# Kernel tuning notes

Hardware: AMD Instinct MI355X
Metric: run time of the kernel (lower is better)

Reference implementation:

```python
import jax, jax.numpy as jnp
import numpy as np

B, NQ, NK, D, H, DR, MLPD = 32, 32, 4096, 256, 8, 2, 2048
ID = D // DR  # internal dim for downsampled cross-attention
EPS = 1e-5


def _ln(x, g, b):
    m = jnp.mean(x, -1, keepdims=True)
    v = jnp.mean((x - m) ** 2, -1, keepdims=True)
    return (x - m) / jnp.sqrt(v + EPS) * g + b


def _attn(q, k, v, qw, qb, kw, kb, vw, vb, ow, ob):
    # linear projections (weights stored as [in, out])
    q = q @ qw + qb
    k = k @ kw + kb
    v = v @ vw + vb
    b, nq, c = q.shape
    d = c // H
    qh = q.reshape(b, nq, H, d)
    kh = k.reshape(b, -1, H, d)
    vh = v.reshape(b, -1, H, d)
    scores = jnp.einsum('bqhd,bkhd->bhqk', qh, kh) * (1.0 / np.sqrt(d))
    a = jax.nn.softmax(scores, axis=-1)
    o = jnp.einsum('bhqk,bkhd->bqhd', a, vh).reshape(b, nq, c)
    return o @ ow + ob


def _forward(queries, keys, query_pe,
             sa_qw, sa_qb, sa_kw, sa_kb, sa_vw, sa_vb, sa_ow, sa_ob,
             t2i_qw, t2i_qb, t2i_kw, t2i_kb, t2i_vw, t2i_vb, t2i_ow, t2i_ob,
             i2t_qw, i2t_qb, i2t_kw, i2t_kb, i2t_vw, i2t_vb, i2t_ow, i2t_ob,
             mlp_w1, mlp_b1, mlp_w2, mlp_b2,
             ln1_g, ln1_b, ln2_g, ln2_b, ln3_g, ln3_b, ln4_g, ln4_b):
    # skip_first_layer_pe = False
    queries = queries + query_pe
    attn_out = _attn(queries, queries, queries,
                     sa_qw, sa_qb, sa_kw, sa_kb, sa_vw, sa_vb, sa_ow, sa_ob)
    queries = _ln(queries + attn_out, ln1_g, ln1_b)
    # cross attention: tokens -> image
    q = queries + query_pe
    attn_out = _attn(q, keys, keys,
                     t2i_qw, t2i_qb, t2i_kw, t2i_kb, t2i_vw, t2i_vb, t2i_ow, t2i_ob)
    queries = _ln(queries + attn_out, ln2_g, ln2_b)
    # MLP block (num_layers=1): act(x W1 + b1) W2 + b2, act = ReLU
    mlp_out = jax.nn.relu(queries @ mlp_w1 + mlp_b1) @ mlp_w2 + mlp_b2
    queries = _ln(queries + mlp_out, ln3_g, ln3_b)
    # cross attention: image -> tokens
    q = queries + query_pe
    attn_out = _attn(keys, q, queries,
                     i2t_qw, i2t_qb, i2t_kw, i2t_kb, i2t_vw, i2t_vb, i2t_ow, i2t_ob)
    keys = _ln(keys + attn_out, ln4_g, ln4_b)
    return queries, keys


def setup_inputs() -> dict:
    key = jax.random.key(0)
    ks = iter(jax.random.split(key, 64))
    def w(shape, s=0.02):
        return jax.random.normal(next(ks), shape, jnp.float32) * s
    inp = {
        'queries': w((B, NQ, D), 1.0),
        'keys': w((B, NK, D), 1.0),
        'query_pe': w((B, NQ, D), 1.0),
    }
    for pre, idim in [('sa', D), ('t2i', ID), ('i2t', ID)]:
        inp[pre + '_qw'] = w((D, idim)); inp[pre + '_qb'] = jnp.zeros((idim,), jnp.float32)
        inp[pre + '_kw'] = w((D, idim)); inp[pre + '_kb'] = jnp.zeros((idim,), jnp.float32)
        inp[pre + '_vw'] = w((D, idim)); inp[pre + '_vb'] = jnp.zeros((idim,), jnp.float32)
        inp[pre + '_ow'] = w((idim, D)); inp[pre + '_ob'] = jnp.zeros((D,), jnp.float32)
    inp['mlp_w1'] = w((D, MLPD)); inp['mlp_b1'] = jnp.zeros((MLPD,), jnp.float32)
    inp['mlp_w2'] = w((MLPD, D)); inp['mlp_b2'] = jnp.zeros((D,), jnp.float32)
    for i in range(1, 5):
        inp['ln%d_g' % i] = jnp.ones((D,), jnp.float32)
        inp['ln%d_b' % i] = jnp.zeros((D,), jnp.float32)
    return inp


def reference(queries, keys, query_pe,
              sa_qw, sa_qb, sa_kw, sa_kb, sa_vw, sa_vb, sa_ow, sa_ob,
              t2i_qw, t2i_qb, t2i_kw, t2i_kb, t2i_vw, t2i_vb, t2i_ow, t2i_ob,
              i2t_qw, i2t_qb, i2t_kw, i2t_kb, i2t_vw, i2t_vb, i2t_ow, i2t_ob,
              mlp_w1, mlp_b1, mlp_w2, mlp_b2,
              ln1_g, ln1_b, ln2_g, ln2_b, ln3_g, ln3_b, ln4_g, ln4_b):
    return _forward(queries, keys, query_pe,
                    sa_qw, sa_qb, sa_kw, sa_kb, sa_vw, sa_vb, sa_ow, sa_ob,
                    t2i_qw, t2i_qb, t2i_kw, t2i_kb, t2i_vw, t2i_vb, t2i_ow, t2i_ob,
                    i2t_qw, i2t_qb, i2t_kw, i2t_kb, i2t_vw, i2t_vb, i2t_ow, i2t_ob,
                    mlp_w1, mlp_b1, mlp_w2, mlp_b2,
                    ln1_g, ln1_b, ln2_g, ln2_b, ln3_g, ln3_b, ln4_g, ln4_b)
```

## Files before the change

### kernel.cpp

```cpp
#include <hip/hip_runtime.h>

typedef unsigned short u16;
typedef __attribute__((ext_vector_type(8))) short s16x8;
typedef __attribute__((ext_vector_type(4))) float f32x4;
typedef __attribute__((ext_vector_type(8))) unsigned short u16x8;

__device__ __forceinline__ float b2f(u16 u) {
  union { unsigned int i; float f; } v; v.i = ((unsigned int)u) << 16; return v.f;
}
__device__ __forceinline__ u16 f2b(float f) {
  union { float f; unsigned int i; } v; v.f = f;
  unsigned int r = v.i + 0x7FFFu + ((v.i >> 16) & 1u);
  return (u16)(r >> 16);
}
__device__ __forceinline__ int pk2(float a, float b) {
  return (int)f2b(a) | ((int)f2b(b) << 16);
}

template<bool RELU>
__global__ void __launch_bounds__(256) k_gemm(
    const u16* __restrict__ A, const u16* __restrict__ Wt,
    const float* __restrict__ bias, u16* __restrict__ C, int N, int K)
{
  __shared__ int4 smem4[2048];
  char* AsB = (char*)smem4;
  char* WsB = (char*)smem4 + 16384;
  const int t = threadIdx.x;
  const int lane = t & 63, wid = t >> 6;
  const int wm = wid >> 1, wn = wid & 1;
  const int l16 = lane & 15, lhi = lane >> 4;
  const int bCol = blockIdx.x * 128;
  const int bRow = blockIdx.y * 128;

  f32x4 acc[4][4];
#pragma unroll
  for (int i = 0; i < 4; ++i)
#pragma unroll
    for (int j = 0; j < 4; ++j) acc[i][j] = (f32x4){0.f, 0.f, 0.f, 0.f};

  const int nk = K >> 6;
  for (int kt = 0; kt < nk; ++kt) {
    const int k0 = kt << 6;
    int4 av[4], wv[4];
#pragma unroll
    for (int i = 0; i < 4; ++i) {
      int L = i * 4096 + t * 16;
      int r = L >> 7, cl = (L >> 4) & 7;
      av[i] = *(const int4*)(A + (size_t)(bRow + r) * K + k0 + cl * 8);
      wv[i] = *(const int4*)(Wt + (size_t)(bCol + r) * K + k0 + cl * 8);
    }
    if (kt) __syncthreads();
#pragma unroll
    for (int i = 0; i < 4; ++i) {
      int L = i * 4096 + t * 16;
      int r = L >> 7, cl = (L >> 4) & 7;
      int off = r * 128 + ((cl ^ (r & 7)) << 4);
      *(int4*)(AsB + off) = av[i];
      *(int4*)(WsB + off) = wv[i];
    }
    __syncthreads();
#pragma unroll
    for (int kk = 0; kk < 2; ++kk) {
      s16x8 af[4], bfr[4];
#pragma unroll
      for (int mt = 0; mt < 4; ++mt) {
        int r = wm * 64 + mt * 16 + l16;
        int ch = kk * 4 + lhi;
        af[mt] = *(const s16x8*)(AsB + r * 128 + ((ch ^ (r & 7)) << 4));
      }
#pragma unroll
      for (int nt = 0; nt < 4; ++nt) {
        int r = wn * 64 + nt * 16 + l16;
        int ch = kk * 4 + lhi;
        bfr[nt] = *(const s16x8*)(WsB + r * 128 + ((ch ^ (r & 7)) << 4));
      }
#pragma unroll
      for (int mt = 0; mt < 4; ++mt)
#pragma unroll
        for (int nt = 0; nt < 4; ++nt)
          acc[mt][nt] = __builtin_amdgcn_mfma_f32_16x16x32_bf16(
              af[mt], bfr[nt], acc[mt][nt], 0, 0, 0);
    }
  }
#pragma unroll
  for (int mt = 0; mt < 4; ++mt) {
#pragma unroll
    for (int nt = 0; nt < 4; ++nt) {
      int cg = bCol + wn * 64 + nt * 16 + l16;
      float bv = bias[cg];
#pragma unroll
      for (int rg = 0; rg < 4; ++rg) {
        int rgl = bRow + wm * 64 + mt * 16 + lhi * 4 + rg;
        float v = acc[mt][nt][rg] + bv;
        if (RELU) v = fmaxf(v, 0.f);
        C[(size_t)rgl * N + cg] = f2b(v);
      }
    }
  }
}

__global__ void __launch_bounds__(256) k_qphase1(
    const float* __restrict__ queries, const float* __restrict__ qpe,
    const u16* __restrict__ Wqkv,
    const float* __restrict__ bqkv,
    const u16* __restrict__ Wo,
    const float* __restrict__ ob,
    const float* __restrict__ g1, const float* __restrict__ b1,
    const u16* __restrict__ Wq2,
    const float* __restrict__ qb2,
    float* __restrict__ q1f, u16* __restrict__ qt)
{
  __shared__ float q0f[32][260];
  __shared__ u16 qkv[32][776];
  __shared__ u16 atb[32][264];
  __shared__ float rs[32][4], rq[32][4];
  const int b = blockIdx.x;
  const int t = threadIdx.x;
  const int lane = t & 63, w = t >> 6;
  const int l16 = lane & 15, lhi = lane >> 4;

  {
    const float4* qg = (const float4*)(queries + (size_t)b * 8192);
    const float4* pg = (const float4*)(qpe + (size_t)b * 8192);
    for (int i = t; i < 2048; i += 256) {
      int row = i >> 6, c4 = (i & 63) * 4;
      float4 qv = qg[i], pv = pg[i];
      *(float4*)&q0f[row][c4] =
          (float4){qv.x + pv.x, qv.y + pv.y, qv.z + pv.z, qv.w + pv.w};
    }
  }
  __syncthreads();

  {
    f32x4 acc[2][12];
#pragma unroll
    for (int i = 0; i < 2; ++i)
#pragma unroll
      for (int j = 0; j < 12; ++j) acc[i][j] = (f32x4){0.f, 0.f, 0.f, 0.f};
#pragma unroll
    for (int kk = 0; kk < 8; ++kk) {
      const int ko = kk * 32 + lhi * 8;
      s16x8 af[2], bfr[12];
#pragma unroll
      for (int mt = 0; mt < 2; ++mt) {
        const float* ap = &q0f[mt * 16 + l16][ko];
        float4 x = *(const float4*)ap;
        float4 y = *(const float4*)(ap + 4);
        int4 p = (int4){pk2(x.x, x.y), pk2(x.z, x.w),
                        pk2(y.x, y.y), pk2(y.z, y.w)};
        af[mt] = *(s16x8*)&p;
      }
#pragma unroll
      for (int nt = 0; nt < 12; ++nt) {
        int row = w * 192 + nt * 16 + l16;
        bfr[nt] = *(const s16x8*)(Wqkv + (size_t)row * 256 + ko);
      }
#pragma unroll
      for (int mt = 0; mt < 2; ++mt)
#pragma unroll
        for (int nt = 0; nt < 12; ++nt)
          acc[mt][nt] = __builtin_amdgcn_mfma_f32_16x16x32_bf16(
              af[mt], bfr[nt], acc[mt][nt], 0, 0, 0);
    }
#pragma unroll
    for (int mt = 0; mt < 2; ++mt)
#pragma unroll
      for (int nt = 0; nt < 12; ++nt) {
        int cg = w * 192 + nt * 16 + l16;
        float bv = bqkv[cg];
#pragma unroll
        for (int rg = 0; rg < 4; ++rg)
          qkv[mt * 16 + lhi * 4 + rg][cg] = f2b(acc[mt][nt][rg] + bv);
      }
  }
  __syncthreads();

  {
    int q = t >> 3, h = t & 7;
    float Qh[32];
#pragma unroll
    for (int c = 0; c < 4; ++c) {
      u16x8 v = *(const u16x8*)&qkv[q][h * 32 + c * 8];
#pragma unroll
      for (int e = 0; e < 8; ++e) Qh[c * 8 + e] = b2f(v[e]);
    }
    float s[32], mx = -INFINITY;
#pragma unroll 4
    for (int j = 0; j < 32; ++j) {
      float a = 0.f;
#pragma unroll
      for (int c = 0; c < 4; ++c) {
        u16x8 v = *(const u16x8*)&qkv[j][256 + h * 32 + c * 8];
#pragma unroll
        for (int e = 0; e < 8; ++e) a += Qh[c * 8 + e] * b2f(v[e]);
      }
      s[j] = a * 0.17677669529663687f;
      mx = fmaxf(mx, s[j]);
    }
    float sum = 0.f;
#pragma unroll
    for (int j = 0; j < 32; ++j) { s[j] = __expf(s[j] - mx); sum += s[j]; }
    float o[32];
#pragma unroll
    for (int d = 0; d < 32; ++d) o[d] = 0.f;
#pragma unroll 4
    for (int j = 0; j < 32; ++j) {
      float p = s[j];
#pragma unroll
      for (int c = 0; c < 4; ++c) {
        u16x8 v = *(const u16x8*)&qkv[j][512 + h * 32 + c * 8];
#pragma unroll
        for (int e = 0; e < 8; ++e) o[c * 8 + e] += p * b2f(v[e]);
      }
    }
    float inv = 1.f / sum;
#pragma unroll
    for (int d = 0; d < 32; ++d) atb[q][h * 32 + d] = f2b(o[d] * inv);
  }
  __syncthreads();

  float yv[2][4][4];
  {
    f32x4 acc[2][4];
#pragma unroll
    for (int i = 0; i < 2; ++i)
#pragma unroll
      for (int j = 0; j < 4; ++j) acc[i][j] = (f32x4){0.f, 0.f, 0.f, 0.f};
#pragma unroll
    for (int kk = 0; kk < 8; ++kk) {
      const int ko = kk * 32 + lhi * 8;
      s16x8 af[2], bfr[4];
#pragma unroll
      for (int mt = 0; mt < 2; ++mt)
        af[mt] = *(const s16x8*)&atb[mt * 16 + l16][ko];
#pragma unroll
      for (int nt = 0; nt < 4; ++nt) {
        int row = w * 64 + nt * 16 + l16;
        bfr[nt] = *(const s16x8*)(Wo + (size_t)row * 256 + ko);
      }
#pragma unroll
      for (int mt = 0; mt < 2; ++mt)
#pragma unroll
        for (int nt = 0; nt < 4; ++nt)
          acc[mt][nt] = __builtin_amdgcn_mfma_f32_16x16x32_bf16(
              af[mt], bfr[nt], acc[mt][nt], 0, 0, 0);
    }
#pragma unroll
    for (int mt = 0; mt < 2; ++mt) {
#pragma unroll
      for (int rg = 0; rg < 4; ++rg) {
        int row = mt * 16 + lhi * 4 + rg;
        float ps = 0.f, pq = 0.f;
#pragma unroll
        for (int nt = 0; nt < 4; ++nt) {
          int cg = w * 64 + nt * 16 + l16;
          float v = acc[mt][nt][rg] + ob[cg] + q0f[row][cg];
          yv[mt][nt][rg] = v;
          ps += v; pq += v * v;
        }
#pragma unroll
        for (int msk = 1; msk < 16; msk <<= 1) {
          ps += __shfl_xor(ps, msk);
          pq += __shfl_xor(pq, msk);
        }
        if (l16 == 0) { rs[row][w] = ps; rq[row][w] = pq; }
      }
    }
  }
  __syncthreads();
  {
#pragma unroll
    for (int mt = 0; mt < 2; ++mt) {
#pragma unroll
      for (int rg = 0; rg < 4; ++rg) {
        int row = mt * 16 + lhi * 4 + rg;
        float ts = rs[row][0] + rs[row][1] + rs[row][2] + rs[row][3];
        float tq = rq[row][0] + rq[row][1] + rq[row][2] + rq[row][3];
        float mean = ts * (1.f / 256.f);
        float var = tq * (1.f / 256.f) - mean * mean;
        float rstd = rsqrtf(var + 1e-5f);
#pragma unroll
        for (int nt = 0; nt < 4; ++nt) {
          int cg = w * 64 + nt * 16 + l16;
          float y = (yv[mt][nt][rg] - mean) * rstd * g1[cg] + b1[cg];
          size_t gi = ((size_t)b * 32 + row) * 256 + cg;
          q1f[gi] = y;
          atb[row][cg] = f2b(y + qpe[gi]);
        }
      }
    }
  }
  __syncthreads();

  {
    f32x4 acc[2][2];
#pragma unroll
    for (int i = 0; i < 2; ++i)
#pragma unroll
      for (int j = 0; j < 2; ++j) acc[i][j] = (f32x4){0.f, 0.f, 0.f, 0.f};
#pragma unroll
    for (int kk = 0; kk < 8; ++kk) {
      const int ko = kk * 32 + lhi * 8;
      s16x8 af[2], bfr[2];
#pragma unroll
      for (int mt = 0; mt < 2; ++mt)
        af[mt] = *(const s16x8*)&atb[mt * 16 + l16][ko];
#pragma unroll
      for (int nt = 0; nt < 2; ++nt) {
        int row = w * 32 + nt * 16 + l16;
        bfr[nt] = *(const s16x8*)(Wq2 + (size_t)row * 256 + ko);
      }
#pragma unroll
      for (int mt = 0; mt < 2; ++mt)
#pragma unroll
        for (int nt = 0; nt < 2; ++nt)
          acc[mt][nt] = __builtin_amdgcn_mfma_f32_16x16x32_bf16(
              af[mt], bfr[nt], acc[mt][nt], 0, 0, 0);
    }
#pragma unroll
    for (int mt = 0; mt < 2; ++mt)
#pragma unroll
      for (int nt = 0; nt < 2; ++nt) {
        int cg = w * 32 + nt * 16 + l16;
        float bv = qb2[cg];
#pragma unroll
        for (int rg = 0; rg < 4; ++rg) {
          int row = mt * 16 + lhi * 4 + rg;
          qt[((size_t)b * 32 + row) * 128 + cg] = f2b(acc[mt][nt][rg] + bv);
        }
      }
  }
}

__global__ void __launch_bounds__(512, 2) k_gemm_kvq(
    const float* __restrict__ A, const u16* __restrict__ Wt,
    const float* __restrict__ bias, u16* __restrict__ KV, u16* __restrict__ QB)
{
  __shared__ char smem[49152];
  char* AsB = smem;
  const int t = threadIdx.x;
  const int lane = t & 63, wid = t >> 6;
  const int wm = wid >> 2, wn = wid & 3;
  const int l16 = lane & 15, lhi = lane >> 4;
  const int bRow = blockIdx.x * 128;

  f32x4 acc[4][6];
#pragma unroll
  for (int i = 0; i < 4; ++i)
#pragma unroll
    for (int j = 0; j < 6; ++j) acc[i][j] = (f32x4){0.f, 0.f, 0.f, 0.f};

  for (int kt = 0; kt < 4; ++kt) {
    const int k0 = kt << 6;
    float4 a0r[2], a1r[2];
#pragma unroll
    for (int i = 0; i < 2; ++i) {
      int L = i * 8192 + t * 16;
      int r = L >> 7, cl = (L >> 4) & 7;
      const float* Af = A + (size_t)(bRow + r) * 256 + k0 + cl * 8;
      a0r[i] = *(const float4*)Af;
      a1r[i] = *(const float4*)(Af + 4);
    }
    if (kt) __syncthreads();
#pragma unroll
    for (int i = 0; i < 2; ++i) {
      int L = i * 8192 + t * 16;
      int r = L >> 7, cl = (L >> 4) & 7;
      int4 p = (int4){pk2(a0r[i].x, a0r[i].y), pk2(a0r[i].z, a0r[i].w),
                      pk2(a1r[i].x, a1r[i].y), pk2(a1r[i].z, a1r[i].w)};
      *(int4*)(AsB + r * 128 + ((cl ^ (r & 7)) << 4)) = p;
    }
    __syncthreads();
#pragma unroll
    for (int kk = 0; kk < 2; ++kk) {
      s16x8 af[4], bfr[6];
#pragma unroll
      for (int nt = 0; nt < 6; ++nt) {
        int row = wn * 96 + nt * 16 + l16;
        bfr[nt] = *(const s16x8*)(Wt + (size_t)row * 256 + k0 + kk * 32 + lhi * 8);
      }
#pragma unroll
      for (int mt = 0; mt < 4; ++mt) {
        int r = wm * 64 + mt * 16 + l16;
        int ch = kk * 4 + lhi;
        af[mt] = *(const s16x8*)(AsB + r * 128 + ((ch ^ (r & 7)) << 4));
      }
#pragma unroll
      for (int mt = 0; mt < 4; ++mt)
#pragma unroll
        for (int nt = 0; nt < 6; ++nt)
          acc[mt][nt] = __builtin_amdgcn_mfma_f32_16x16x32_bf16(
              af[mt], bfr[nt], acc[mt][nt], 0, 0, 0);
    }
  }
  u16* ldsO = (u16*)smem;
  for (int half = 0; half < 2; ++half) {
    __syncthreads();
    if (wm == half) {
#pragma unroll
      for (int mt = 0; mt < 4; ++mt) {
#pragma unroll
        for (int nt = 0; nt < 6; ++nt) {
          int cg = wn * 96 + nt * 16 + l16;
          float bv = bias[cg];
#pragma unroll
          for (int rg = 0; rg < 4; ++rg) {
            int r = mt * 16 + lhi * 4 + rg;
            ldsO[r * 384 + cg] = f2b(acc[mt][nt][rg] + bv);
          }
        }
      }
    }
    __syncthreads();
#pragma unroll
    for (int i = 0; i < 6; ++i) {
      int chunk = i * 512 + t;
      int r = chunk / 48, c8 = chunk - r * 48;
      int row = bRow + half * 64 + r;
      int4 v = *(int4*)(ldsO + r * 384 + c8 * 8);
      if (c8 < 32) *(int4*)(KV + (size_t)row * 256 + c8 * 8) = v;
      else         *(int4*)(QB + (size_t)row * 128 + (c8 - 32) * 8) = v;
    }
  }
}

__global__ void __launch_bounds__(256) k_gemm_ln(
    const u16* __restrict__ A, const u16* __restrict__ Wt,
    const float* __restrict__ bias, const float* __restrict__ res,
    const float* __restrict__ g, const float* __restrict__ bl,
    float* __restrict__ out)
{
  __shared__ int4 smem4[512];
  __shared__ float rsum[2][32][2], rsq[2][32][2];
  char* AsB = (char*)smem4;
  const int t = threadIdx.x;
  const int lane = t & 63, wid = t >> 6;
  const int wm = wid >> 1, wn = wid & 1;
  const int l16 = lane & 15, lhi = lane >> 4;
  const int bRow = blockIdx.x * 64;

  f32x4 acc[2][8];
#pragma unroll
  for (int i = 0; i < 2; ++i)
#pragma unroll
    for (int j = 0; j < 8; ++j) acc[i][j] = (f32x4){0.f, 0.f, 0.f, 0.f};

  for (int kt = 0; kt < 2; ++kt) {
    const int k0 = kt << 6;
    int4 av[2];
#pragma unroll
    for (int i = 0; i < 2; ++i) {
      int L = i * 4096 + t * 16;
      int r = L >> 7, cl = (L >> 4) & 7;
      av[i] = *(const int4*)(A + (size_t)(bRow + r) * 128 + k0 + cl * 8);
    }
    if (kt) __syncthreads();
#pragma unroll
    for (int i = 0; i < 2; ++i) {
      int L = i * 4096 + t * 16;
      int r = L >> 7, cl = (L >> 4) & 7;
      *(int4*)(AsB + r * 128 + ((cl ^ (r & 7)) << 4)) = av[i];
    }
    __syncthreads();
#pragma unroll
    for (int kk = 0; kk < 2; ++kk) {
      s16x8 af[2], bfr[8];
#pragma unroll
      for (int nt = 0; nt < 8; ++nt) {
        int row = wn * 128 + nt * 16 + l16;
        bfr[nt] = *(const s16x8*)(Wt + (size_t)row * 128 + k0 + kk * 32 + lhi * 8);
      }
#pragma unroll
      for (int mt = 0; mt < 2; ++mt) {
        int r = wm * 32 + mt * 16 + l16;
        int ch = kk * 4 + lhi;
        af[mt] = *(const s16x8*)(AsB + r * 128 + ((ch ^ (r & 7)) << 4));
      }
#pragma unroll
      for (int mt = 0; mt < 2; ++mt)
#pragma unroll
        for (int nt = 0; nt < 8; ++nt)
          acc[mt][nt] = __builtin_amdgcn_mfma_f32_16x16x32_bf16(
              af[mt], bfr[nt], acc[mt][nt], 0, 0, 0);
    }
  }
#pragma unroll
  for (int mt = 0; mt < 2; ++mt) {
#pragma unroll
    for (int nt = 0; nt < 8; ++nt) {
      int cg = wn * 128 + nt * 16 + l16;
      float bv = bias[cg];
#pragma unroll
      for (int rg = 0; rg < 4; ++rg) {
        int row = bRow + wm * 32 + mt * 16 + lhi * 4 + rg;
        acc[mt][nt][rg] += bv + res[(size_t)row * 256 + cg];
      }
    }
  }
#pragma unroll
  for (int mt = 0; mt < 2; ++mt) {
#pragma unroll
    for (int rg = 0; rg < 4; ++rg) {
      float ps = 0.f, pq = 0.f;
#pragma unroll
      for (int nt = 0; nt < 8; ++nt) {
        float v = acc[mt][nt][rg];
        ps += v; pq += v * v;
      }
#pragma unroll
      for (int msk = 1; msk < 16; msk <<= 1) {
        ps += __shfl_xor(ps, msk);
        pq += __shfl_xor(pq, msk);
      }
      if (l16 == 0) {
        int rl = mt * 16 + lhi * 4 + rg;
        rsum[wm][rl][wn] = ps;
        rsq[wm][rl][wn] = pq;
      }
    }
  }
  __syncthreads();
#pragma unroll
  for (int mt = 0; mt < 2; ++mt) {
#pragma unroll
    for (int rg = 0; rg < 4; ++rg) {
      int rl = mt * 16 + lhi * 4 + rg;
      float ts = rsum[wm][rl][0] + rsum[wm][rl][1];
      float tq = rsq[wm][rl][0] + rsq[wm][rl][1];
      float mean = ts * (1.f / 256.f);
      float var = tq * (1.f / 256.f) - mean * mean;
      float rstd = rsqrtf(var + 1e-5f);
      int row = bRow + wm * 32 + rl;
#pragma unroll
      for (int nt = 0; nt < 8; ++nt) {
        int cg = wn * 128 + nt * 16 + l16;
        out[(size_t)row * 256 + cg] =
            (acc[mt][nt][rg] - mean) * rstd * g[cg] + bl[cg];
      }
    }
  }
}

struct TDesc { const float* src; void* dst; int K; int N; int mode; int blk0; };
struct TArgs { TDesc d[24]; int n; };

__global__ void __launch_bounds__(256) k_trans(TArgs a)
{
  int blk = blockIdx.x;
  int i = 0;
  while (i + 1 < a.n && blk >= a.d[i + 1].blk0) ++i;
  TDesc td = a.d[i];
  int e = (blk - td.blk0) * 256 + threadIdx.x;
  int tot = td.K * td.N;
  if (e >= tot) return;
  if (td.mode == 0) {
    int k = e / td.N, n = e - k * td.N;
    ((u16*)td.dst)[(size_t)n * td.K + k] = f2b(td.src[e]);
  } else {
    ((float*)td.dst)[e] = td.src[e];
  }
}

__global__ void __launch_bounds__(128) k_attn_t2i_part(
    const u16* __restrict__ Qt, const u16* __restrict__ KV,
    float* __restrict__ part)
{
  __shared__ int4 kvs[4096];
  int c = blockIdx.x, b = blockIdx.y;
  int tid = threadIdx.x;
  const int4* src = (const int4*)(KV + ((size_t)b * 4096 + c * 128) * 256);
  for (int i = tid; i < 4096; i += 128) kvs[i] = src[i];
  __syncthreads();
  int qp = tid >> 3, h = tid & 7;
  const u16* lds = (const u16*)kvs;

  float q0[16], q1[16];
  {
    const u16* p0 = Qt + (size_t)(b * 32 + qp) * 128 + h * 16;
    const u16* p1 = Qt + (size_t)(b * 32 + qp + 16) * 128 + h * 16;
    u16x8 a0 = *(const u16x8*)p0, b0 = *(const u16x8*)(p0 + 8);
    u16x8 a1 = *(const u16x8*)p1, b1 = *(const u16x8*)(p1 + 8);
#pragma unroll
    for (int e = 0; e < 8; ++e) {
      q0[e] = b2f(a0[e]); q0[8 + e] = b2f(b0[e]);
      q1[e] = b2f(a1[e]); q1[8 + e] = b2f(b1[e]);
    }
  }
  float m0 = -INFINITY, s0 = 0.f, m1 = -INFINITY, s1 = 0.f;
  float acc0[16], acc1[16];
#pragma unroll
  for (int d = 0; d < 16; ++d) { acc0[d] = 0.f; acc1[d] = 0.f; }

  for (int j = 0; j < 128; ++j) {
    const u16* kr = lds + j * 256 + h * 16;
    u16x8 ka = *(const u16x8*)kr;
    u16x8 kb = *(const u16x8*)(kr + 8);
    float l0 = 0.f, l1 = 0.f;
#pragma unroll
    for (int e = 0; e < 8; ++e) {
      float klo = b2f(ka[e]), khi = b2f(kb[e]);
      l0 += q0[e] * klo + q0[8 + e] * khi;
      l1 += q1[e] * klo + q1[8 + e] * khi;
    }
    l0 *= 0.25f; l1 *= 0.25f;
    const u16* vr = kr + 128;
    u16x8 va = *(const u16x8*)vr;
    u16x8 vb = *(const u16x8*)(vr + 8);
    float nm0 = fmaxf(m0, l0), nm1 = fmaxf(m1, l1);
    float c0 = __expf(m0 - nm0), p0 = __expf(l0 - nm0);
    float c1 = __expf(m1 - nm1), p1 = __expf(l1 - nm1);
    s0 = s0 * c0 + p0; s1 = s1 * c1 + p1;
#pragma unroll
    for (int e = 0; e < 8; ++e) {
      float vlo = b2f(va[e]), vhi = b2f(vb[e]);
      acc0[e] = acc0[e] * c0 + p0 * vlo;
      acc0[8 + e] = acc0[8 + e] * c0 + p0 * vhi;
      acc1[e] = acc1[e] * c1 + p1 * vlo;
      acc1[8 + e] = acc1[8 + e] * c1 + p1 * vhi;
    }
    m0 = nm0; m1 = nm1;
  }
  float* r0 = part + (((size_t)(b * 32 + qp) * 8 + h) * 32 + c) * 18;
  float* r1 = part + (((size_t)(b * 32 + qp + 16) * 8 + h) * 32 + c) * 18;
#pragma unroll
  for (int d = 0; d < 16; ++d) { r0[d] = acc0[d]; r1[d] = acc1[d]; }
  r0[16] = m0; r0[17] = s0;
  r1[16] = m1; r1[17] = s1;
}

__global__ void __launch_bounds__(256) k_attn_t2i_merge(
    const float* __restrict__ part, u16* __restrict__ out)
{
  int b = blockIdx.x >> 3, h = blockIdx.x & 7;
  int q = threadIdx.x >> 3, ds = threadIdx.x & 7;
  const float* base = part + (((size_t)(b * 32 + q) * 8 + h) * 32) * 18;
  float mg = -INFINITY;
#pragma unroll 4
  for (int c = 0; c < 32; ++c) mg = fmaxf(mg, base[c * 18 + 16]);
  float sg = 0.f, a0 = 0.f, a1 = 0.f;
#pragma unroll 4
  for (int c = 0; c < 32; ++c) {
    const float* rec = base + c * 18;
    float w = __expf(rec[16] - mg);
    sg += rec[17] * w;
    a0 += rec[ds * 2] * w;
    a1 += rec[ds * 2 + 1] * w;
  }
  float inv = 1.f / sg;
  u16* op = out + (size_t)(b * 32 + q) * 128 + h * 16 + ds * 2;
  op[0] = f2b(a0 * inv);
  op[1] = f2b(a1 * inv);
}

__global__ void __launch_bounds__(256) k_attn_i2t(
    const u16* __restrict__ Qb, const u16* __restrict__ Kc,
    const u16* __restrict__ Vc, u16* __restrict__ out)
{
  __shared__ float Kl[32][132], Vl[32][132];
  int blk = blockIdx.x;
  int b = blk >> 7;
  int r0 = (blk & 127) * 32;
  for (int idx = threadIdx.x; idx < 4096; idx += 256) {
    int j = idx >> 7, c = idx & 127;
    Kl[j][c] = b2f(Kc[(size_t)(b * 32 + j) * 128 + c]);
    Vl[j][c] = b2f(Vc[(size_t)(b * 32 + j) * 128 + c]);
  }
  __syncthreads();
  int lr = threadIdx.x >> 3, h = threadIdx.x & 7;
  size_t row = (size_t)b * 4096 + r0 + lr;
  const u16* qp = Qb + row * 128 + h * 16;
  float q[16];
  {
    u16x8 qa = *(const u16x8*)qp;
    u16x8 qb2 = *(const u16x8*)(qp + 8);
#pragma unroll
    for (int e = 0; e < 8; ++e) { q[e] = b2f(qa[e]); q[8 + e] = b2f(qb2[e]); }
  }
  float lg[32];
  float mx = -INFINITY;
#pragma unroll
  for (int j = 0; j < 32; ++j) {
    float a = 0.f;
#pragma unroll
    for (int d = 0; d < 16; ++d) a += q[d] * Kl[j][h * 16 + d];
    lg[j] = a * 0.25f;
    mx = fmaxf(mx, lg[j]);
  }
  float sum = 0.f;
#pragma unroll
  for (int j = 0; j < 32; ++j) { lg[j] = __expf(lg[j] - mx); sum += lg[j]; }
  float acc[16];
#pragma unroll
  for (int d = 0; d < 16; ++d) acc[d] = 0.f;
#pragma unroll
  for (int j = 0; j < 32; ++j) {
    float p = lg[j];
#pragma unroll
    for (int d = 0; d < 16; ++d) acc[d] += p * Vl[j][h * 16 + d];
  }
  float inv = 1.f / sum;
  u16* op = out + row * 128 + h * 16;
#pragma unroll
  for (int d = 0; d < 16; ++d) op[d] = f2b(acc[d] * inv);
}

__global__ void __launch_bounds__(256) k_addln_small(
    const float* __restrict__ res, const u16* __restrict__ delta,
    const float* __restrict__ g, const float* __restrict__ bb,
    float* outf, u16* outb, const float* pe, u16* outpe)
{
  int row = blockIdx.x * 4 + (threadIdx.x >> 6);
  int lane = threadIdx.x & 63;
  size_t base = (size_t)row * 256 + lane * 4;
  float4 xv = *(const float4*)(res + base);
  ushort4 dv = *(const ushort4*)(delta + base);
  float v0 = xv.x + b2f(dv.x), v1 = xv.y + b2f(dv.y);
  float v2 = xv.z + b2f(dv.z), v3 = xv.w + b2f(dv.w);
  float sum = v0 + v1 + v2 + v3;
  float sq = v0 * v0 + v1 * v1 + v2 * v2 + v3 * v3;
#pragma unroll
  for (int msk = 1; msk < 64; msk <<= 1) {
    sum += __shfl_xor(sum, msk);
    sq += __shfl_xor(sq, msk);
  }
  float mean = sum * (1.f / 256.f);
  float var = sq * (1.f / 256.f) - mean * mean;
  float rstd = rsqrtf(var + 1e-5f);
  float4 gv = *(const float4*)(g + lane * 4);
  float4 bv = *(const float4*)(bb + lane * 4);
  float y0 = (v0 - mean) * rstd * gv.x + bv.x;
  float y1 = (v1 - mean) * rstd * gv.y + bv.y;
  float y2 = (v2 - mean) * rstd * gv.z + bv.z;
  float y3 = (v3 - mean) * rstd * gv.w + bv.w;
  if (outf) { float4 o{y0, y1, y2, y3}; *(float4*)(outf + base) = o; }
  if (outb) {
    ushort4 o{f2b(y0), f2b(y1), f2b(y2), f2b(y3)};
    *(ushort4*)(outb + base) = o;
  }
  if (outpe) {
    float4 pv = *(const float4*)(pe + base);
    ushort4 o{f2b(y0 + pv.x), f2b(y1 + pv.y), f2b(y2 + pv.z), f2b(y3 + pv.w)};
    *(ushort4*)(outpe + base) = o;
  }
}

extern "C" void kernel_launch(void* const* d_in, const int* in_sizes, int n_in,
                              void* d_out, int out_size, void* d_ws, size_t ws_size,
                              hipStream_t stream)
{
  (void)in_sizes; (void)n_in; (void)out_size; (void)ws_size;
  const float* queries = (const float*)d_in[0];
  const float* keys    = (const float*)d_in[1];
  const float* qpe     = (const float*)d_in[2];
  const float* sa_qw = (const float*)d_in[3];  const float* sa_qb = (const float*)d_in[4];
  const float* sa_kw = (const float*)d_in[5];  const float* sa_kb = (const float*)d_in[6];
  const float* sa_vw = (const float*)d_in[7];  const float* sa_vb = (const float*)d_in[8];
  const float* sa_ow = (const float*)d_in[9];  const float* sa_ob = (const float*)d_in[10];
  const float* t2i_qw = (const float*)d_in[11]; const float* t2i_qb = (const float*)d_in[12];
  const float* t2i_kw = (const float*)d_in[13]; const float* t2i_kb = (const float*)d_in[14];
  const float* t2i_vw = (const float*)d_in[15]; const float* t2i_vb = (const float*)d_in[16];
  const float* t2i_ow = (const float*)d_in[17]; const float* t2i_ob = (const float*)d_in[18];
  const float* i2t_qw = (const float*)d_in[19]; const float* i2t_qb = (const float*)d_in[20];
  const float* i2t_kw = (const float*)d_in[21]; const float* i2t_kb = (const float*)d_in[22];
  const float* i2t_vw = (const float*)d_in[23]; const float* i2t_vb = (const float*)d_in[24];
  const float* i2t_ow = (const float*)d_in[25]; const float* i2t_ob = (const float*)d_in[26];
  const float* mlp_w1 = (const float*)d_in[27]; const float* mlp_b1 = (const float*)d_in[28];
  const float* mlp_w2 = (const float*)d_in[29]; const float* mlp_b2 = (const float*)d_in[30];
  const float* ln1_g = (const float*)d_in[31]; const float* ln1_b = (const float*)d_in[32];
  const float* ln2_g = (const float*)d_in[33]; const float* ln2_b = (const float*)d_in[34];
  const float* ln3_g = (const float*)d_in[35]; const float* ln3_b = (const float*)d_in[36];
  const float* ln4_g = (const float*)d_in[37]; const float* ln4_b = (const float*)d_in[38];

  float* out_q = (float*)d_out;
  float* out_k = out_q + 262144;

  u16* kvbuf  = (u16*)out_k;
  u16* qb_big = (u16*)out_k + 33554432;
  float* t2i_part = (float*)((u16*)out_k + 50331648);

  char* ws = (char*)d_ws;
  size_t off = 0;
  auto alloc = [&](size_t bytes) -> char* {
    char* p = ws + off;
    off += (bytes + 255) & ~(size_t)255;
    return p;
  };
  u16* wt_saqkv = (u16*)alloc(768 * 256 * 2);
  u16* wt_saow  = (u16*)alloc(256 * 256 * 2);
  u16* wt_t2iq  = (u16*)alloc(128 * 256 * 2);
  u16* wt_kvq   = (u16*)alloc(384 * 256 * 2);
  u16* wt_t2io  = (u16*)alloc(256 * 128 * 2);
  u16* wt_i2tk  = (u16*)alloc(128 * 256 * 2);
  u16* wt_i2tv  = (u16*)alloc(128 * 256 * 2);
  u16* wt_i2to  = (u16*)alloc(256 * 128 * 2);
  u16* wt_w1    = (u16*)alloc(2048 * 256 * 2);
  u16* wt_w2    = (u16*)alloc(256 * 2048 * 2);
  float* b_saqkv = (float*)alloc(768 * 4);
  float* b_kvq   = (float*)alloc(384 * 4);
  float* q1f = (float*)alloc(262144 * 4);
  float* q2f = (float*)alloc(262144 * 4);
  u16* qt    = (u16*)alloc(131072 * 2);
  u16* at2   = (u16*)alloc(131072 * 2);
  u16* o2    = (u16*)alloc(262144 * 2);
  u16* q2b   = (u16*)alloc(262144 * 2);
  u16* hbuf  = (u16*)alloc(2097152 * 2);
  u16* mo    = (u16*)alloc(262144 * 2);
  u16* q3b   = (u16*)alloc(262144 * 2);
  u16* q3pe  = (u16*)alloc(262144 * 2);
  u16* kc    = (u16*)alloc(131072 * 2);
  u16* vc    = (u16*)alloc(131072 * 2);
  u16* ab_big = (u16*)alloc((size_t)16777216 * 2);

  TArgs ta{};
  int nb = 0, id = 0;
  auto addT = [&](const float* s, void* d, int K, int N, int mode) {
    ta.d[id].src = s; ta.d[id].dst = d; ta.d[id].K = K; ta.d[id].N = N;
    ta.d[id].mode = mode; ta.d[id].blk0 = nb;
    nb += (K * N + 255) / 256;
    ++id;
  };
  addT(sa_qw, wt_saqkv, 256, 256, 0);
  addT(sa_kw, wt_saqkv + 256 * 256, 256, 256, 0);
  addT(sa_vw, wt_saqkv + 512 * 256, 256, 256, 0);
  addT(sa_ow, wt_saow, 256, 256, 0);
  addT(t2i_qw, wt_t2iq, 256, 128, 0);
  addT(t2i_kw, wt_kvq, 256, 128, 0);
  addT(t2i_vw, wt_kvq + 128 * 256, 256, 128, 0);
  addT(i2t_qw, wt_kvq + 256 * 256, 256, 128, 0);
  addT(t2i_ow, wt_t2io, 128, 256, 0);
  addT(i2t_kw, wt_i2tk, 256, 128, 0);
  addT(i2t_vw, wt_i2tv, 256, 128, 0);
  addT(i2t_ow, wt_i2to, 128, 256, 0);
  addT(mlp_w1, wt_w1, 256, 2048, 0);
  addT(mlp_w2, wt_w2, 2048, 256, 0);
  addT(sa_qb, b_saqkv, 1, 256, 1);
  addT(sa_kb, b_saqkv + 256, 1, 256, 1);
  addT(sa_vb, b_saqkv + 512, 1, 256, 1);
  addT(t2i_kb, b_kvq, 1, 128, 1);
  addT(t2i_vb, b_kvq + 128, 1, 128, 1);
  addT(i2t_qb, b_kvq + 256, 1, 128, 1);
  ta.n = id;
  k_trans<<<nb, 256, 0, stream>>>(ta);

  k_qphase1<<<32, 256, 0, stream>>>(queries, qpe, wt_saqkv, b_saqkv,
                                    wt_saow, sa_ob, ln1_g, ln1_b,
                                    wt_t2iq, t2i_qb, q1f, qt);
  k_gemm_kvq<<<1024, 512, 0, stream>>>(keys, wt_kvq, b_kvq, kvbuf, qb_big);
  k_attn_t2i_part<<<dim3(32, 32), 128, 0, stream>>>(qt, kvbuf, t2i_part);
  k_attn_t2i_merge<<<256, 256, 0, stream>>>(t2i_part, at2);
  k_gemm<false><<<dim3(2, 8), 256, 0, stream>>>(at2, wt_t2io, t2i_ob,
                                                o2, 256, 128);
  k_addln_small<<<256, 256, 0, stream>>>(q1f, o2, ln2_g, ln2_b, q2f, q2b,
                                         nullptr, nullptr);
  k_gemm<true><<<dim3(16, 8), 256, 0, stream>>>(q2b, wt_w1, mlp_b1,
                                                hbuf, 2048, 256);
  k_gemm<false><<<dim3(2, 8), 256, 0, stream>>>(hbuf, wt_w2, mlp_b2,
                                                mo, 256, 2048);
  k_addln_small<<<256, 256, 0, stream>>>(q2f, mo, ln3_g, ln3_b, out_q, q3b,
                                         qpe, q3pe);
  k_gemm<false><<<dim3(1, 8), 256, 0, stream>>>(q3pe, wt_i2tk, i2t_kb,
                                                kc, 128, 256);
  k_gemm<false><<<dim3(1, 8), 256, 0, stream>>>(q3b, wt_i2tv, i2t_vb,
                                                vc, 128, 256);
  k_attn_i2t<<<4096, 256, 0, stream>>>(qb_big, kc, vc, ab_big);
  k_gemm_ln<<<2048, 256, 0, stream>>>(ab_big, wt_i2to, i2t_ob, keys,
                                      ln4_g, ln4_b, out_k);
}
```

Before: 550.9 us.

## Fuse t2i out-proj, LN2, MLP, LN3 and i2t K/V projections per batch

Replaces the chain of small GEMM and add-layernorm launches after token-to-image attention with a single per-batch kernel. It computes the output projection, residual plus LN2, the MLP in hidden-dimension chunks staged in LDS, residual plus LN3, and the image-to-token K and V projections. This removes several launches and global round-trips of intermediates. In exchange, the work runs on only 32 blocks, each streaming the full MLP weights from global memory.

Result: faster. 494.2 us (-10.3%).

```diff
diff --git a/kernel.cpp b/kernel.cpp
--- a/kernel.cpp
+++ b/kernel.cpp
@@ -15,88 +15,6 @@
 }
 __device__ __forceinline__ int pk2(float a, float b) {
   return (int)f2b(a) | ((int)f2b(b) << 16);
-}
-
-template<bool RELU>
-__global__ void __launch_bounds__(256) k_gemm(
-    const u16* __restrict__ A, const u16* __restrict__ Wt,
-    const float* __restrict__ bias, u16* __restrict__ C, int N, int K)
-{
-  __shared__ int4 smem4[2048];
-  char* AsB = (char*)smem4;
-  char* WsB = (char*)smem4 + 16384;
-  const int t = threadIdx.x;
-  const int lane = t & 63, wid = t >> 6;
-  const int wm = wid >> 1, wn = wid & 1;
-  const int l16 = lane & 15, lhi = lane >> 4;
-  const int bCol = blockIdx.x * 128;
-  const int bRow = blockIdx.y * 128;
-
-  f32x4 acc[4][4];
-#pragma unroll
-  for (int i = 0; i < 4; ++i)
-#pragma unroll
-    for (int j = 0; j < 4; ++j) acc[i][j] = (f32x4){0.f, 0.f, 0.f, 0.f};
-
-  const int nk = K >> 6;
-  for (int kt = 0; kt < nk; ++kt) {
-    const int k0 = kt << 6;
-    int4 av[4], wv[4];
-#pragma unroll
-    for (int i = 0; i < 4; ++i) {
-      int L = i * 4096 + t * 16;
-      int r = L >> 7, cl = (L >> 4) & 7;
-      av[i] = *(const int4*)(A + (size_t)(bRow + r) * K + k0 + cl * 8);
-      wv[i] = *(const int4*)(Wt + (size_t)(bCol + r) * K + k0 + cl * 8);
-    }
-    if (kt) __syncthreads();
-#pragma unroll
-    for (int i = 0; i < 4; ++i) {
-      int L = i * 4096 + t * 16;
-      int r = L >> 7, cl = (L >> 4) & 7;
-      int off = r * 128 + ((cl ^ (r & 7)) << 4);
-      *(int4*)(AsB + off) = av[i];
-      *(int4*)(WsB + off) = wv[i];
-    }
-    __syncthreads();
-#pragma unroll
-    for (int kk = 0; kk < 2; ++kk) {
-      s16x8 af[4], bfr[4];
-#pragma unroll
-      for (int mt = 0; mt < 4; ++mt) {
-        int r = wm * 64 + mt * 16 + l16;
-        int ch = kk * 4 + lhi;
-        af[mt] = *(const s16x8*)(AsB + r * 128 + ((ch ^ (r & 7)) << 4));
-      }
-#pragma unroll
-      for (int nt = 0; nt < 4; ++nt) {
-        int r = wn * 64 + nt * 16 + l16;
-        int ch = kk * 4 + lhi;
-        bfr[nt] = *(const s16x8*)(WsB + r * 128 + ((ch ^ (r & 7)) << 4));
-      }
-#pragma unroll
-      for (int mt = 0; mt < 4; ++mt)
-#pragma unroll
-        for (int nt = 0; nt < 4; ++nt)
-          acc[mt][nt] = __builtin_amdgcn_mfma_f32_16x16x32_bf16(
-              af[mt], bfr[nt], acc[mt][nt], 0, 0, 0);
-    }
-  }
-#pragma unroll
-  for (int mt = 0; mt < 4; ++mt) {
-#pragma unroll
-    for (int nt = 0; nt < 4; ++nt) {
-      int cg = bCol + wn * 64 + nt * 16 + l16;
-      float bv = bias[cg];
-#pragma unroll
-      for (int rg = 0; rg < 4; ++rg) {
-        int rgl = bRow + wm * 64 + mt * 16 + lhi * 4 + rg;
-        float v = acc[mt][nt][rg] + bv;
-        if (RELU) v = fmaxf(v, 0.f);
-        C[(size_t)rgl * N + cg] = f2b(v);
-      }
-    }
-  }
 }
 
 __global__ void __launch_bounds__(256) k_qphase1(
@@ -332,6 +250,279 @@
   }
 }
 
+__global__ void __launch_bounds__(256) k_qphase2(
+    const u16* __restrict__ at2,
+    const float* __restrict__ q1f,
+    const u16* __restrict__ Wo2,
+    const float* __restrict__ ob2,
+    const float* __restrict__ g2, const float* __restrict__ b2v,
+    const u16* __restrict__ W1,
+    const float* __restrict__ bb1,
+    const u16* __restrict__ W2,
+    const float* __restrict__ bb2,
+    const float* __restrict__ g3, const float* __restrict__ b3v,
+    const float* __restrict__ qpe,
+    const u16* __restrict__ Wk,
+    const float* __restrict__ kb,
+    const u16* __restrict__ Wv,
+    const float* __restrict__ vbv,
+    float* __restrict__ out_q, u16* __restrict__ kc, u16* __restrict__ vc)
+{
+  __shared__ u16 atb[32][136];
+  __shared__ float q2f[32][260];
+  __shared__ u16 q2b[32][264];
+  __shared__ u16 hb[32][520];
+  __shared__ u16 yb[32][264];
+  __shared__ u16 ypeb[32][264];
+  __shared__ float rs[32][4], rq[32][4];
+  const int b = blockIdx.x;
+  const int t = threadIdx.x;
+  const int lane = t & 63, w = t >> 6;
+  const int l16 = lane & 15, lhi = lane >> 4;
+
+  {
+    const int4* src = (const int4*)(at2 + (size_t)b * 32 * 128);
+    for (int i = t; i < 512; i += 256) {
+      int r = i >> 4, c8 = i & 15;
+      *(int4*)&atb[r][c8 * 8] = src[i];
+    }
+  }
+  __syncthreads();
+
+  {
+    f32x4 acc[2][4];
+#pragma unroll
+    for (int i = 0; i < 2; ++i)
+#pragma unroll
+      for (int j = 0; j < 4; ++j) acc[i][j] = (f32x4){0.f, 0.f, 0.f, 0.f};
+#pragma unroll
+    for (int kk = 0; kk < 4; ++kk) {
+      const int ko = kk * 32 + lhi * 8;
+      s16x8 af[2], bfr[4];
+#pragma unroll
+      for (int mt = 0; mt < 2; ++mt)
+        af[mt] = *(const s16x8*)&atb[mt * 16 + l16][ko];
+#pragma unroll
+      for (int nt = 0; nt < 4; ++nt) {
+        int row = w * 64 + nt * 16 + l16;
+        bfr[nt] = *(const s16x8*)(Wo2 + (size_t)row * 128 + ko);
+      }
+#pragma unroll
+      for (int mt = 0; mt < 2; ++mt)
+#pragma unroll
+        for (int nt = 0; nt < 4; ++nt)
+          acc[mt][nt] = __builtin_amdgcn_mfma_f32_16x16x32_bf16(
+              af[mt], bfr[nt], acc[mt][nt], 0, 0, 0);
+    }
+    float yv[2][4][4];
+#pragma unroll
+    for (int mt = 0; mt < 2; ++mt) {
+#pragma unroll
+      for (int rg = 0; rg < 4; ++rg) {
+        int row = mt * 16 + lhi * 4 + rg;
+        float ps = 0.f, pq = 0.f;
+#pragma unroll
+        for (int nt = 0; nt < 4; ++nt) {
+          int cg = w * 64 + nt * 16 + l16;
+          float v = acc[mt][nt][rg] + ob2[cg] +
+                    q1f[((size_t)b * 32 + row) * 256 + cg];
+          yv[mt][nt][rg] = v;
+          ps += v; pq += v * v;
+        }
+#pragma unroll
+        for (int msk = 1; msk < 16; msk <<= 1) {
+          ps += __shfl_xor(ps, msk);
+          pq += __shfl_xor(pq, msk);
+        }
+        if (l16 == 0) { rs[row][w] = ps; rq[row][w] = pq; }
+      }
+    }
+    __syncthreads();
+#pragma unroll
+    for (int mt = 0; mt < 2; ++mt) {
+#pragma unroll
+      for (int rg = 0; rg < 4; ++rg) {
+        int row = mt * 16 + lhi * 4 + rg;
+        float ts = rs[row][0] + rs[row][1] + rs[row][2] + rs[row][3];
+        float tq = rq[row][0] + rq[row][1] + rq[row][2] + rq[row][3];
+        float mean = ts * (1.f / 256.f);
+        float var = tq * (1.f / 256.f) - mean * mean;
+        float rstd = rsqrtf(var + 1e-5f);
+#pragma unroll
+        for (int nt = 0; nt < 4; ++nt) {
+          int cg = w * 64 + nt * 16 + l16;
+          float y = (yv[mt][nt][rg] - mean) * rstd * g2[cg] + b2v[cg];
+          q2f[row][cg] = y;
+          q2b[row][cg] = f2b(y);
+        }
+      }
+    }
+  }
+  __syncthreads();
+
+  f32x4 oacc[2][4];
+#pragma unroll
+  for (int i = 0; i < 2; ++i)
+#pragma unroll
+    for (int j = 0; j < 4; ++j) oacc[i][j] = (f32x4){0.f, 0.f, 0.f, 0.f};
+  for (int hc = 0; hc < 4; ++hc) {
+    f32x4 a1[2][8];
+#pragma unroll
+    for (int i = 0; i < 2; ++i)
+#pragma unroll
+      for (int j = 0; j < 8; ++j) a1[i][j] = (f32x4){0.f, 0.f, 0.f, 0.f};
+#pragma unroll
+    for (int kk = 0; kk < 8; ++kk) {
+      const int ko = kk * 32 + lhi * 8;
+      s16x8 af[2], bfr[8];
+#pragma unroll
+      for (int mt = 0; mt < 2; ++mt)
+        af[mt] = *(const s16x8*)&q2b[mt * 16 + l16][ko];
+#pragma unroll
+      for (int nt = 0; nt < 8; ++nt) {
+        int row = hc * 512 + w * 128 + nt * 16 + l16;
+        bfr[nt] = *(const s16x8*)(W1 + (size_t)row * 256 + ko);
+      }
+#pragma unroll
+      for (int mt = 0; mt < 2; ++mt)
+#pragma unroll
+        for (int nt = 0; nt < 8; ++nt)
+          a1[mt][nt] = __builtin_amdgcn_mfma_f32_16x16x32_bf16(
+              af[mt], bfr[nt], a1[mt][nt], 0, 0, 0);
+    }
+    if (hc) __syncthreads();
+#pragma unroll
+    for (int mt = 0; mt < 2; ++mt)
+#pragma unroll
+      for (int nt = 0; nt < 8; ++nt) {
+        int cg = w * 128 + nt * 16 + l16;
+        float bv = bb1[hc * 512 + cg];
+#pragma unroll
+        for (int rg = 0; rg < 4; ++rg)
+          hb[mt * 16 + lhi * 4 + rg][cg] =
+              f2b(fmaxf(a1[mt][nt][rg] + bv, 0.f));
+      }
+    __syncthreads();
+#pragma unroll
+    for (int kk2 = 0; kk2 < 16; ++kk2) {
+      const int ko = kk2 * 32 + lhi * 8;
+      s16x8 af[2], bfr[4];
+#pragma unroll
+      for (int mt = 0; mt < 2; ++mt)
+        af[mt] = *(const s16x8*)&hb[mt * 16 + l16][ko];
+#pragma unroll
+      for (int nt = 0; nt < 4; ++nt) {
+        int row = w * 64 + nt * 16 + l16;
+        bfr[nt] = *(const s16x8*)(W2 + (size_t)row * 2048 + hc * 512 + ko);
+      }
+#pragma unroll
+      for (int mt = 0; mt < 2; ++mt)
+#pragma unroll
+        for (int nt = 0; nt < 4; ++nt)
+          oacc[mt][nt] = __builtin_amdgcn_mfma_f32_16x16x32_bf16(
+              af[mt], bfr[nt], oacc[mt][nt], 0, 0, 0);
+    }
+  }
+
+  {
+    float yv[2][4][4];
+#pragma unroll
+    for (int mt = 0; mt < 2; ++mt) {
+#pragma unroll
+      for (int rg = 0; rg < 4; ++rg) {
+        int row = mt * 16 + lhi * 4 + rg;
+        float ps = 0.f, pq = 0.f;
+#pragma unroll
+        for (int nt = 0; nt < 4; ++nt) {
+          int cg = w * 64 + nt * 16 + l16;
+          float v = oacc[mt][nt][rg] + bb2[cg] + q2f[row][cg];
+          yv[mt][nt][rg] = v;
+          ps += v; pq += v * v;
+        }
+#pragma unroll
+        for (int msk = 1; msk < 16; msk <<= 1) {
+          ps += __shfl_xor(ps, msk);
+          pq += __shfl_xor(pq, msk);
+        }
+        if (l16 == 0) { rs[row][w] = ps; rq[row][w] = pq; }
+      }
+    }
+    __syncthreads();
+#pragma unroll
+    for (int mt = 0; mt < 2; ++mt) {
+#pragma unroll
+      for (int rg = 0; rg < 4; ++rg) {
+        int row = mt * 16 + lhi * 4 + rg;
+        float ts = rs[row][0] + rs[row][1] + rs[row][2] + rs[row][3];
+        float tq = rq[row][0] + rq[row][1] + rq[row][2] + rq[row][3];
+        float mean = ts * (1.f / 256.f);
+        float var = tq * (1.f / 256.f) - mean * mean;
+        float rstd = rsqrtf(var + 1e-5f);
+#pragma unroll
+        for (int nt = 0; nt < 4; ++nt) {
+          int cg = w * 64 + nt * 16 + l16;
+          float y = (yv[mt][nt][rg] - mean) * rstd * g3[cg] + b3v[cg];
+          size_t gi = ((size_t)b * 32 + row) * 256 + cg;
+          out_q[gi] = y;
+          yb[row][cg] = f2b(y);
+          ypeb[row][cg] = f2b(y + qpe[gi]);
+        }
+      }
+    }
+  }
+  __syncthreads();
+
+  {
+    f32x4 ak[2][2], av[2][2];
+#pragma unroll
+    for (int i = 0; i < 2; ++i)
+#pragma unroll
+      for (int j = 0; j < 2; ++j) {
+        ak[i][j] = (f32x4){0.f, 0.f, 0.f, 0.f};
+        av[i][j] = (f32x4){0.f, 0.f, 0.f, 0.f};
+      }
+#pragma unroll
+    for (int kk = 0; kk < 8; ++kk) {
+      const int ko = kk * 32 + lhi * 8;
+      s16x8 afk[2], afv[2], bk[2], bv2[2];
+#pragma unroll
+      for (int mt = 0; mt < 2; ++mt) {
+        afk[mt] = *(const s16x8*)&ypeb[mt * 16 + l16][ko];
+        afv[mt] = *(const s16x8*)&yb[mt * 16 + l16][ko];
+      }
+#pragma unroll
+      for (int nt = 0; nt < 2; ++nt) {
+        int row = w * 32 + nt * 16 + l16;
+        bk[nt] = *(const s16x8*)(Wk + (size_t)row * 256 + ko);
+        bv2[nt] = *(const s16x8*)(Wv + (size_t)row * 256 + ko);
+      }
+#pragma unroll
+      for (int mt = 0; mt < 2; ++mt)
+#pragma unroll
+        for (int nt = 0; nt < 2; ++nt) {
+          ak[mt][nt] = __builtin_amdgcn_mfma_f32_16x16x32_bf16(
+              afk[mt], bk[nt], ak[mt][nt], 0, 0, 0);
+          av[mt][nt] = __builtin_amdgcn_mfma_f32_16x16x32_bf16(
+              afv[mt], bv2[nt], av[mt][nt], 0, 0, 0);
+        }
+    }
+#pragma unroll
+    for (int mt = 0; mt < 2; ++mt)
+#pragma unroll
+      for (int nt = 0; nt < 2; ++nt) {
+        int cg = w * 32 + nt * 16 + l16;
+        float kbv = kb[cg], vbb = vbv[cg];
+#pragma unroll
+        for (int rg = 0; rg < 4; ++rg) {
+          int row = mt * 16 + lhi * 4 + rg;
+          size_t gi = ((size_t)b * 32 + row) * 128 + cg;
+          kc[gi] = f2b(ak[mt][nt][rg] + kbv);
+          vc[gi] = f2b(av[mt][nt][rg] + vbb);
+        }
+      }
+  }
+}
+
 __global__ void __launch_bounds__(512, 2) k_gemm_kvq(
     const float* __restrict__ A, const u16* __restrict__ Wt,
     const float* __restrict__ bias, u16* __restrict__ KV, u16* __restrict__ QB)
@@ -702,46 +893,6 @@
   u16* op = out + row * 128 + h * 16;
 #pragma unroll
   for (int d = 0; d < 16; ++d) op[d] = f2b(acc[d] * inv);
-}
-
-__global__ void __launch_bounds__(256) k_addln_small(
-    const float* __restrict__ res, const u16* __restrict__ delta,
-    const float* __restrict__ g, const float* __restrict__ bb,
-    float* outf, u16* outb, const float* pe, u16* outpe)
-{
-  int row = blockIdx.x * 4 + (threadIdx.x >> 6);
-  int lane = threadIdx.x & 63;
-  size_t base = (size_t)row * 256 + lane * 4;
-  float4 xv = *(const float4*)(res + base);
-  ushort4 dv = *(const ushort4*)(delta + base);
-  float v0 = xv.x + b2f(dv.x), v1 = xv.y + b2f(dv.y);
-  float v2 = xv.z + b2f(dv.z), v3 = xv.w + b2f(dv.w);
-  float sum = v0 + v1 + v2 + v3;
-  float sq = v0 * v0 + v1 * v1 + v2 * v2 + v3 * v3;
-#pragma unroll
-  for (int msk = 1; msk < 64; msk <<= 1) {
-    sum += __shfl_xor(sum, msk);
-    sq += __shfl_xor(sq, msk);
-  }
-  float mean = sum * (1.f / 256.f);
-  float var = sq * (1.f / 256.f) - mean * mean;
-  float rstd = rsqrtf(var + 1e-5f);
-  float4 gv = *(const float4*)(g + lane * 4);
-  float4 bv = *(const float4*)(bb + lane * 4);
-  float y0 = (v0 - mean) * rstd * gv.x + bv.x;
-  float y1 = (v1 - mean) * rstd * gv.y + bv.y;
-  float y2 = (v2 - mean) * rstd * gv.z + bv.z;
-  float y3 = (v3 - mean) * rstd * gv.w + bv.w;
-  if (outf) { float4 o{y0, y1, y2, y3}; *(float4*)(outf + base) = o; }
-  if (outb) {
-    ushort4 o{f2b(y0), f2b(y1), f2b(y2), f2b(y3)};
-    *(ushort4*)(outb + base) = o;
-  }
-  if (outpe) {
-    float4 pv = *(const float4*)(pe + base);
-    ushort4 o{f2b(y0 + pv.x), f2b(y1 + pv.y), f2b(y2 + pv.z), f2b(y3 + pv.w)};
-    *(ushort4*)(outpe + base) = o;
-  }
 }
 
 extern "C" void kernel_launch(void* const* d_in, const int* in_sizes, int n_in,
@@ -798,15 +949,8 @@
   float* b_saqkv = (float*)alloc(768 * 4);
   float* b_kvq   = (float*)alloc(384 * 4);
   float* q1f = (float*)alloc(262144 * 4);
-  float* q2f = (float*)alloc(262144 * 4);
   u16* qt    = (u16*)alloc(131072 * 2);
   u16* at2   = (u16*)alloc(131072 * 2);
-  u16* o2    = (u16*)alloc(262144 * 2);
-  u16* q2b   = (u16*)alloc(262144 * 2);
-  u16* hbuf  = (u16*)alloc(2097152 * 2);
-  u16* mo    = (u16*)alloc(262144 * 2);
-  u16* q3b   = (u16*)alloc(262144 * 2);
-  u16* q3pe  = (u16*)alloc(262144 * 2);
   u16* kc    = (u16*)alloc(131072 * 2);
   u16* vc    = (u16*)alloc(131072 * 2);
   u16* ab_big = (u16*)alloc((size_t)16777216 * 2);
@@ -848,20 +992,11 @@
   k_gemm_kvq<<<1024, 512, 0, stream>>>(keys, wt_kvq, b_kvq, kvbuf, qb_big);
   k_attn_t2i_part<<<dim3(32, 32), 128, 0, stream>>>(qt, kvbuf, t2i_part);
   k_attn_t2i_merge<<<256, 256, 0, stream>>>(t2i_part, at2);
-  k_gemm<false><<<dim3(2, 8), 256, 0, stream>>>(at2, wt_t2io, t2i_ob,
-                                                o2, 256, 128);
-  k_addln_small<<<256, 256, 0, stream>>>(q1f, o2, ln2_g, ln2_b, q2f, q2b,
-                                         nullptr, nullptr);
-  k_gemm<true><<<dim3(16, 8), 256, 0, stream>>>(q2b, wt_w1, mlp_b1,
-                                                hbuf, 2048, 256);
-  k_gemm<false><<<dim3(2, 8), 256, 0, stream>>>(hbuf, wt_w2, mlp_b2,
-                                                mo, 256, 2048);
-  k_addln_small<<<256, 256, 0, stream>>>(q2f, mo, ln3_g, ln3_b, out_q, q3b,
-                                         qpe, q3pe);
-  k_gemm<false><<<dim3(1, 8), 256, 0, stream>>>(q3pe, wt_i2tk, i2t_kb,
-                                                kc, 128, 256);
-  k_gemm<false><<<dim3(1, 8), 256, 0, stream>>>(q3b, wt_i2tv, i2t_vb,
-                                                vc, 128, 256);
+  k_qphase2<<<32, 256, 0, stream>>>(at2, q1f, wt_t2io, t2i_ob, ln2_g, ln2_b,
+                                    wt_w1, mlp_b1, wt_w2, mlp_b2,
+                                    ln3_g, ln3_b, qpe,
+                                    wt_i2tk, i2t_kb, wt_i2tv, i2t_vb,
+                                    out_q, kc, vc);
   k_attn_i2t<<<4096, 256, 0, stream>>>(qb_big, kc, vc, ab_big);
   k_gemm_ln<<<2048, 256, 0, stream>>>(ab_big, wt_i2to, i2t_ob, keys,
                                       ln4_g, ln4_b, out_k);
```
